# Optimization experiments

Measured on AMD Instinct MI355X. Metric: run time of the kernel, lower is better.

## Reference

```python
import jax, jax.numpy as jnp
import numpy as np

# dims
B, S = 1, 32768          # batch, grid seqlen (32^3 latent grid)
NQ, NE = 32768, 262144   # mesh query nodes, grid->query edges
IN, EMB, HID, BOT, PREDH, OUT, NDIM = 192, 192, 192, 192, 192, 4, 3
MAX_WAVELENGTH = 10000.0


def sincos_embed(coords, dim, ndim):
    # ContinuousSincosEmbed: dim % ndim == 0 and (dim//ndim) even here -> no padding
    eff = dim // ndim                                     # 64 dims per coordinate
    omega = 1.0 / MAX_WAVELENGTH ** (jnp.arange(0, eff, 2, dtype=jnp.float32) / eff)  # [eff//2]
    out = coords[..., None] * omega                       # [N, ndim, eff//2]
    emb = jnp.concatenate([jnp.sin(out), jnp.cos(out)], axis=-1)  # [N, ndim, eff]
    return emb.reshape(coords.shape[0], ndim * eff)       # [N, dim]


def _linear_params(key, fan_in, fan_out):
    k1, k2 = jax.random.split(key)
    lim = 1.0 / np.sqrt(fan_in)
    w = jax.random.uniform(k1, (fan_in, fan_out), jnp.float32, -lim, lim)
    b = jax.random.uniform(k2, (fan_out,), jnp.float32, -lim, lim)
    return w, b


def setup_inputs() -> dict:
    key = jax.random.key(0)
    ks = jax.random.split(key, 10)
    x = jax.random.normal(ks[0], (B, S, IN), jnp.float32)
    query_pos = jax.random.uniform(ks[1], (NQ, NDIM), jnp.float32) * 100.0
    # edges sorted by query index (required by the CSR segment reduce in the original)
    qidx = jnp.sort(jax.random.randint(ks[2], (NE,), 0, NQ))
    gidx = jax.random.randint(ks[3], (NE,), 0, B * S)
    grid_to_query_edges = jnp.stack([qidx, gidx], axis=1).astype(jnp.int64)
    proj_w, proj_b = _linear_params(ks[4], IN, EMB)
    msg0_w, msg0_b = _linear_params(ks[5], 2 * EMB, 2 * HID)
    msg1_w, msg1_b = _linear_params(ks[6], 2 * HID, 2 * HID)
    msg2_w, msg2_b = _linear_params(ks[7], 2 * HID, BOT)
    pred0_w, pred0_b = _linear_params(ks[8], BOT, PREDH)
    pred1_w, pred1_b = _linear_params(ks[9], PREDH, OUT)
    return dict(x=x, query_pos=query_pos, grid_to_query_edges=grid_to_query_edges,
                proj_w=proj_w, proj_b=proj_b,
                msg0_w=msg0_w, msg0_b=msg0_b, msg1_w=msg1_w, msg1_b=msg1_b,
                msg2_w=msg2_w, msg2_b=msg2_b,
                pred0_w=pred0_w, pred0_b=pred0_b, pred1_w=pred1_w, pred1_b=pred1_b)


def reference(x, query_pos, grid_to_query_edges,
              proj_w, proj_b, msg0_w, msg0_b, msg1_w, msg1_b, msg2_w, msg2_b,
              pred0_w, pred0_b, pred1_w, pred1_b):
    gelu = lambda t: jax.nn.gelu(t, approximate=False)  # torch nn.GELU default (erf)
    # flatten grid tokens and project
    xf = x.reshape(-1, x.shape[-1]) @ proj_w + proj_b          # [B*S, EMB]
    qe = sincos_embed(query_pos, EMB, NDIM)                    # [NQ, EMB]
    qidx = grid_to_query_edges[:, 0]
    gidx = grid_to_query_edges[:, 1]
    # gather + concat per edge
    h = jnp.concatenate([xf[gidx], qe[qidx]], axis=1)          # [NE, 2*EMB]
    # message MLP
    h = gelu(h @ msg0_w + msg0_b)
    h = gelu(h @ msg1_w + msg1_b)
    h = h @ msg2_w + msg2_b                                    # [NE, BOT]
    # segment mean to query nodes (empty segments -> 0, matching segment_csr mean)
    nq = query_pos.shape[0]
    seg_sum = jax.ops.segment_sum(h, qidx, num_segments=nq)    # [NQ, BOT]
    cnt = jax.ops.segment_sum(jnp.ones((qidx.shape[0], 1), h.dtype), qidx, num_segments=nq)
    m = seg_sum / jnp.maximum(cnt, 1.0)
    # prediction head
    out = gelu(m @ pred0_w + pred0_b) @ pred1_w + pred1_b      # [NQ, OUT]
    return out
```

## Files before the change

### kernel.cpp

```cpp
#include <hip/hip_runtime.h>
#include <math.h>

#define N_Q    32768
#define N_E    262144

typedef _Float16 half8 __attribute__((ext_vector_type(8)));
typedef _Float16 half4v __attribute__((ext_vector_type(4)));
typedef float f32x4 __attribute__((ext_vector_type(4)));

__device__ __forceinline__ float gelu_f(float x) {
    float ax = fabsf(x);
    float t = __builtin_amdgcn_rcpf(fmaf(0.33269070724668f, ax, 1.0f));
    float poly = t * fmaf(t, fmaf(t, 0.7478556f, -0.0958798f), 0.3480242f);
    float e = exp2f(-0.72134752044448f * ax * ax);
    float u = fmaf(-poly, e, 1.0f);
    return 0.5f * fmaf(ax, u, x);
}

__global__ __launch_bounds__(256) void embed_kernel(const float* __restrict__ qpos,
                                                    _Float16* __restrict__ qe) {
    int gid = blockIdx.x * 256 + threadIdx.x;
    int q = gid / 96, r = gid - q * 96;
    int d = r >> 5, i = r & 31;
    float omega = exp2f(-(float)i * 0.41524101186092029f);
    float arg = qpos[q * 3 + d] * omega;
    float rev = arg * 0.15915494309189535f;
    rev = rev - floorf(rev);
    float s = __builtin_amdgcn_sinf(rev);
    float c = __builtin_amdgcn_cosf(rev);
    int base = q * 192 + d * 64 + i;
    qe[base] = (_Float16)s;
    qe[base + 32] = (_Float16)c;
}

__device__ __forceinline__ void pack_one(const float* __restrict__ W,
                                         _Float16* __restrict__ Wp,
                                         int K, int N, int blk0, int tid) {
    int u = blk0 * 256 + tid;
    if (u * 8 >= K * N) return;
    int l = u & 63, blk = u >> 6;
    int nks = K >> 5;
    int ntile = blk / nks, ks = blk - ntile * nks;
    int n = ntile * 16 + (l & 15);
    int k0 = ks * 32 + (l >> 4) * 8;
    half8 v;
    #pragma unroll
    for (int j = 0; j < 8; ++j) v[j] = (_Float16)W[(size_t)(k0 + j) * N + n];
    *(half8*)(Wp + (size_t)u * 8) = v;
}

__global__ __launch_bounds__(256) void pack_all_kernel(
    const float* __restrict__ pw,  _Float16* __restrict__ WpP,
    const float* __restrict__ m0,  _Float16* __restrict__ Wp0,
    const float* __restrict__ m1,  _Float16* __restrict__ Wp1,
    const float* __restrict__ m2,  _Float16* __restrict__ Wp2,
    const float* __restrict__ hw,  _Float16* __restrict__ WpH) {
    int b = blockIdx.x, t = threadIdx.x;
    if      (b < 18)  pack_one(pw, WpP, 192, 192, b,        t);
    else if (b < 90)  pack_one(m0, Wp0, 384, 384, b - 18,   t);
    else if (b < 162) pack_one(m1, Wp1, 384, 384, b - 90,   t);
    else if (b < 198) pack_one(m2, Wp2, 384, 192, b - 162,  t);
    else              pack_one(hw, WpH, 192, 192, b - 198,  t);
}

#define PK 200

__global__ __launch_bounds__(256, 2) void proj_mfma_kernel(
    const float* __restrict__ x, const _Float16* __restrict__ Wp,
    const float* __restrict__ bias, _Float16* __restrict__ xf)
{
    __shared__ _Float16 hA[64 * PK];
    const int t = threadIdx.x;
    const int r0 = blockIdx.x * 64;
    const int lane = t & 63;
    const int w = t >> 6;
    const int ln = lane & 15, lq = lane >> 4;

    #pragma unroll
    for (int i = 0; i < 12; ++i) {
        int idx = t + 256 * i;
        int r = idx / 48, c4 = idx - r * 48;
        float4 v = ((const float4*)(x + (size_t)(r0 + r) * 192))[c4];
        half4v hv; hv[0] = (_Float16)v.x; hv[1] = (_Float16)v.y;
        hv[2] = (_Float16)v.z; hv[3] = (_Float16)v.w;
        *(half4v*)(hA + r * PK + c4 * 4) = hv;
    }
    __syncthreads();

    f32x4 acc[4][3];
    #pragma unroll
    for (int nt = 0; nt < 3; ++nt) {
        float bv = bias[w * 48 + nt * 16 + ln];
        #pragma unroll
        for (int mt = 0; mt < 4; ++mt) acc[mt][nt] = (f32x4){bv, bv, bv, bv};
    }
    #pragma unroll 2
    for (int ks = 0; ks < 6; ++ks) {
        half8 a[4], bf[3];
        #pragma unroll
        for (int mt = 0; mt < 4; ++mt)
            a[mt] = *(const half8*)(hA + (mt * 16 + ln) * PK + ks * 32 + lq * 8);
        #pragma unroll
        for (int nt = 0; nt < 3; ++nt)
            bf[nt] = *(const half8*)(Wp + (size_t)(((w * 3 + nt) * 6 + ks) * 512 + lane * 8));
        #pragma unroll
        for (int nt = 0; nt < 3; ++nt)
            #pragma unroll
            for (int mt = 0; mt < 4; ++mt)
                acc[mt][nt] = __builtin_amdgcn_mfma_f32_16x16x32_f16(a[mt], bf[nt], acc[mt][nt], 0, 0, 0);
    }
    #pragma unroll
    for (int mt = 0; mt < 4; ++mt)
        #pragma unroll
        for (int nt = 0; nt < 3; ++nt)
            #pragma unroll
            for (int r = 0; r < 4; ++r) {
                int m = mt * 16 + lq * 4 + r;
                int n = w * 48 + nt * 16 + ln;
                xf[(size_t)(r0 + m) * 192 + n] = (_Float16)acc[mt][nt][r];
            }
}

#define PADK 392

__global__ __launch_bounds__(512, 6) void edge_mlp_kernel(
    const _Float16* __restrict__ xf, const _Float16* __restrict__ qe,
    const int* __restrict__ edges,
    const _Float16* __restrict__ Wp0, const float* __restrict__ b0,
    const _Float16* __restrict__ Wp1, const float* __restrict__ b1,
    const _Float16* __restrict__ Wp2, const float* __restrict__ b2,
    float* __restrict__ seg, float* __restrict__ cnt)
{
    __shared__ _Float16 hA[64 * PADK];
    __shared__ int qi[64], gi[64];
    float* h2 = (float*)hA;

    const int t = threadIdx.x;
    const int e0 = blockIdx.x * 64;
    const int lane = t & 63;
    const int w = t >> 6;
    const int ln = lane & 15;
    const int lq = lane >> 4;

    if (t < 64) {
        qi[t] = edges[2 * (e0 + t)];
        gi[t] = edges[2 * (e0 + t) + 1];
    }
    __syncthreads();

    #pragma unroll
    for (int i = 0; i < 6; ++i) {
        int idx = t + 512 * i;
        int m = idx / 48, c = idx - m * 48;
        const half8* src = (c < 24) ? ((const half8*)(xf + (size_t)gi[m] * 192) + c)
                                    : ((const half8*)(qe + (size_t)qi[m] * 192) + (c - 24));
        *(half8*)(hA + m * PADK + c * 8) = *src;
    }
    __syncthreads();

    #pragma unroll 1
    for (int L = 0; L < 2; ++L) {
        const _Float16* __restrict__ Wp = L ? Wp1 : Wp0;
        const float* __restrict__ bias = L ? b1 : b0;

        f32x4 acc[4][3];
        #pragma unroll
        for (int nt = 0; nt < 3; ++nt) {
            float bv = bias[w * 48 + nt * 16 + ln];
            #pragma unroll
            for (int mt = 0; mt < 4; ++mt)
                acc[mt][nt] = (f32x4){bv, bv, bv, bv};
        }
        #pragma unroll 2
        for (int ks = 0; ks < 12; ++ks) {
            half8 a[4], bf[3];
            #pragma unroll
            for (int mt = 0; mt < 4; ++mt)
                a[mt] = *(const half8*)(hA + (mt * 16 + ln) * PADK + ks * 32 + lq * 8);
            #pragma unroll
            for (int nt = 0; nt < 3; ++nt)
                bf[nt] = *(const half8*)(Wp + (size_t)(((w * 3 + nt) * 12 + ks) * 512 + lane * 8));
            #pragma unroll
            for (int nt = 0; nt < 3; ++nt)
                #pragma unroll
                for (int mt = 0; mt < 4; ++mt)
                    acc[mt][nt] = __builtin_amdgcn_mfma_f32_16x16x32_f16(a[mt], bf[nt], acc[mt][nt], 0, 0, 0);
        }
        __syncthreads();
        #pragma unroll
        for (int mt = 0; mt < 4; ++mt)
            #pragma unroll
            for (int nt = 0; nt < 3; ++nt)
                #pragma unroll
                for (int r = 0; r < 4; ++r) {
                    int m = mt * 16 + lq * 4 + r;
                    int n = w * 48 + nt * 16 + ln;
                    hA[m * PADK + n] = (_Float16)gelu_f(acc[mt][nt][r]);
                }
        __syncthreads();
    }

    {
        const int n0 = (w & 3) * 48;
        const int mh = (w >> 2) * 2;
        f32x4 acc[2][3];
        #pragma unroll
        for (int nt = 0; nt < 3; ++nt) {
            float bv = b2[n0 + nt * 16 + ln];
            #pragma unroll
            for (int mt = 0; mt < 2; ++mt)
                acc[mt][nt] = (f32x4){bv, bv, bv, bv};
        }
        #pragma unroll 2
        for (int ks = 0; ks < 12; ++ks) {
            half8 a[2], bf[3];
            #pragma unroll
            for (int mt = 0; mt < 2; ++mt)
                a[mt] = *(const half8*)(hA + ((mh + mt) * 16 + ln) * PADK + ks * 32 + lq * 8);
            #pragma unroll
            for (int nt = 0; nt < 3; ++nt)
                bf[nt] = *(const half8*)(Wp2 + (size_t)((((w & 3) * 3 + nt) * 12 + ks) * 512 + lane * 8));
            #pragma unroll
            for (int nt = 0; nt < 3; ++nt)
                #pragma unroll
                for (int mt = 0; mt < 2; ++mt)
                    acc[mt][nt] = __builtin_amdgcn_mfma_f32_16x16x32_f16(a[mt], bf[nt], acc[mt][nt], 0, 0, 0);
        }
        __syncthreads();
        #pragma unroll
        for (int mt = 0; mt < 2; ++mt)
            #pragma unroll
            for (int nt = 0; nt < 3; ++nt)
                #pragma unroll
                for (int r = 0; r < 4; ++r) {
                    int m = (mh + mt) * 16 + lq * 4 + r;
                    int n = n0 + nt * 16 + ln;
                    h2[m * 192 + n] = acc[mt][nt][r];
                }
        __syncthreads();
    }

    if (t < 384) {
        int half = t >= 192;
        int col = t - half * 192;
        int mlo = half * 32, mhi = mlo + 32;
        float a = 0.0f;
        for (int m = mlo; m < mhi; ++m) {
            a += h2[m * 192 + col];
            if (m == mhi - 1 || qi[m + 1] != qi[m]) {
                atomicAdd(&seg[(size_t)qi[m] * 192 + col], a);
                a = 0.0f;
            }
        }
    } else if (t < 386) {
        int half = t - 384;
        int mlo = half * 32, mhi = mlo + 32;
        float run = 1.0f;
        for (int m = mlo + 1; m < mhi; ++m) {
            if (qi[m] != qi[m - 1]) { atomicAdd(&cnt[qi[m - 1]], run); run = 1.0f; }
            else run += 1.0f;
        }
        atomicAdd(&cnt[qi[mhi - 1]], run);
    }
}

#define PSK 196

__global__ __launch_bounds__(256, 2) void head_kernel(
    const float* __restrict__ seg, const float* __restrict__ cnt,
    const _Float16* __restrict__ Wp0, const float* __restrict__ b0,
    const float* __restrict__ w1, const float* __restrict__ b1,
    float* __restrict__ out)
{
    __shared__ _Float16 hA[64 * PK];
    __shared__ float ps[64 * PSK];
    __shared__ float w1s[192 * 4];
    __shared__ float invc[64];
    const int t = threadIdx.x;
    const int r0 = blockIdx.x * 64;
    const int lane = t & 63;
    const int w = t >> 6;
    const int ln = lane & 15, lq = lane >> 4;

    if (t < 64) invc[t] = 1.0f / fmaxf(cnt[r0 + t], 1.0f);
    if (t < 192) ((float4*)w1s)[t] = ((const float4*)w1)[t];
    __syncthreads();

    #pragma unroll
    for (int i = 0; i < 12; ++i) {
        int idx = t + 256 * i;
        int r = idx / 48, c4 = idx - r * 48;
        float inv = invc[r];
        float4 v = ((const float4*)(seg + (size_t)(r0 + r) * 192))[c4];
        half4v hv; hv[0] = (_Float16)(v.x * inv); hv[1] = (_Float16)(v.y * inv);
        hv[2] = (_Float16)(v.z * inv); hv[3] = (_Float16)(v.w * inv);
        *(half4v*)(hA + r * PK + c4 * 4) = hv;
    }
    __syncthreads();

    f32x4 acc[4][3];
    #pragma unroll
    for (int nt = 0; nt < 3; ++nt) {
        float bv = b0[w * 48 + nt * 16 + ln];
        #pragma unroll
        for (int mt = 0; mt < 4; ++mt) acc[mt][nt] = (f32x4){bv, bv, bv, bv};
    }
    #pragma unroll 2
    for (int ks = 0; ks < 6; ++ks) {
        half8 a[4], bf[3];
        #pragma unroll
        for (int mt = 0; mt < 4; ++mt)
            a[mt] = *(const half8*)(hA + (mt * 16 + ln) * PK + ks * 32 + lq * 8);
        #pragma unroll
        for (int nt = 0; nt < 3; ++nt)
            bf[nt] = *(const half8*)(Wp0 + (size_t)(((w * 3 + nt) * 6 + ks) * 512 + lane * 8));
        #pragma unroll
        for (int nt = 0; nt < 3; ++nt)
            #pragma unroll
            for (int mt = 0; mt < 4; ++mt)
                acc[mt][nt] = __builtin_amdgcn_mfma_f32_16x16x32_f16(a[mt], bf[nt], acc[mt][nt], 0, 0, 0);
    }
    #pragma unroll
    for (int mt = 0; mt < 4; ++mt)
        #pragma unroll
        for (int nt = 0; nt < 3; ++nt)
            #pragma unroll
            for (int r = 0; r < 4; ++r) {
                int m = mt * 16 + lq * 4 + r;
                int n = w * 48 + nt * 16 + ln;
                ps[m * PSK + n] = gelu_f(acc[mt][nt][r]);
            }
    __syncthreads();

    {
        int r = t >> 2, oo = t & 3;
        float a = b1[oo];
        for (int k = 0; k < 192; ++k)
            a = fmaf(ps[r * PSK + k], w1s[k * 4 + oo], a);
        out[(size_t)(r0 + r) * 4 + oo] = a;
    }
}

extern "C" void kernel_launch(void* const* d_in, const int* in_sizes, int n_in,
                              void* d_out, int out_size, void* d_ws, size_t ws_size,
                              hipStream_t stream) {
    (void)in_sizes; (void)n_in; (void)out_size; (void)ws_size;
    const float* x       = (const float*)d_in[0];
    const float* qpos    = (const float*)d_in[1];
    const int*   edges   = (const int*)d_in[2];
    const float* proj_w  = (const float*)d_in[3];
    const float* proj_b  = (const float*)d_in[4];
    const float* msg0_w  = (const float*)d_in[5];
    const float* msg0_b  = (const float*)d_in[6];
    const float* msg1_w  = (const float*)d_in[7];
    const float* msg1_b  = (const float*)d_in[8];
    const float* msg2_w  = (const float*)d_in[9];
    const float* msg2_b  = (const float*)d_in[10];
    const float* pred0_w = (const float*)d_in[11];
    const float* pred0_b = (const float*)d_in[12];
    const float* pred1_w = (const float*)d_in[13];
    const float* pred1_b = (const float*)d_in[14];
    float* out = (float*)d_out;

    char* ws = (char*)d_ws;
    _Float16* xf  = (_Float16*)(ws);
    _Float16* qe  = (_Float16*)(ws + 12582912);
    float*    seg = (float*)(ws + 25165824);
    float*    cnt = (float*)(ws + 50331648);
    _Float16* Wp0 = (_Float16*)(ws + 50462720);
    _Float16* Wp1 = (_Float16*)(ws + 50757632);
    _Float16* Wp2 = (_Float16*)(ws + 51052544);
    _Float16* WpP = (_Float16*)(ws + 51200000);
    _Float16* WpH = (_Float16*)(ws + 51273728);

    hipMemsetAsync(seg, 0, 25165824 + 131072, stream);
    embed_kernel<<<12288, 256, 0, stream>>>(qpos, qe);
    pack_all_kernel<<<216, 256, 0, stream>>>(proj_w, WpP, msg0_w, Wp0,
                                             msg1_w, Wp1, msg2_w, Wp2,
                                             pred0_w, WpH);
    proj_mfma_kernel<<<512, 256, 0, stream>>>(x, WpP, proj_b, xf);
    edge_mlp_kernel<<<4096, 512, 0, stream>>>(xf, qe, edges,
                                              Wp0, msg0_b, Wp1, msg1_b, Wp2, msg2_b,
                                              seg, cnt);
    head_kernel<<<512, 256, 0, stream>>>(seg, cnt, WpH, pred0_b,
                                         pred1_w, pred1_b, out);
}
```

Measured before the change: 372.4 us.

## Fuse prep launches, restructure edge gather, hoist address math, vectorise head dot

Merges the sincos embedding, weight packing and segment-buffer zeroing into a single prep kernel, replacing a memset and two launches. Rewrites the edge-feature gather so each thread copies strided 16-byte chunks of one edge's grid and query rows. Precomputes LDS and weight base pointers in the MFMA loops and epilogues, and vectorises the head's final 192-wide dot product with float4 reads. Intent is to cut launch overhead and per-iteration index arithmetic; the gather layout change may alter coalescing behaviour.

```diff
diff --git a/kernel.cpp b/kernel.cpp
--- a/kernel.cpp
+++ b/kernel.cpp
@@ -15,22 +15,6 @@
     float e = exp2f(-0.72134752044448f * ax * ax);
     float u = fmaf(-poly, e, 1.0f);
     return 0.5f * fmaf(ax, u, x);
-}
-
-__global__ __launch_bounds__(256) void embed_kernel(const float* __restrict__ qpos,
-                                                    _Float16* __restrict__ qe) {
-    int gid = blockIdx.x * 256 + threadIdx.x;
-    int q = gid / 96, r = gid - q * 96;
-    int d = r >> 5, i = r & 31;
-    float omega = exp2f(-(float)i * 0.41524101186092029f);
-    float arg = qpos[q * 3 + d] * omega;
-    float rev = arg * 0.15915494309189535f;
-    rev = rev - floorf(rev);
-    float s = __builtin_amdgcn_sinf(rev);
-    float c = __builtin_amdgcn_cosf(rev);
-    int base = q * 192 + d * 64 + i;
-    qe[base] = (_Float16)s;
-    qe[base + 32] = (_Float16)c;
 }
 
 __device__ __forceinline__ void pack_one(const float* __restrict__ W,
@@ -49,18 +33,43 @@
     *(half8*)(Wp + (size_t)u * 8) = v;
 }
 
-__global__ __launch_bounds__(256) void pack_all_kernel(
+__global__ __launch_bounds__(256) void prep_kernel(
+    const float* __restrict__ qpos, _Float16* __restrict__ qe,
     const float* __restrict__ pw,  _Float16* __restrict__ WpP,
     const float* __restrict__ m0,  _Float16* __restrict__ Wp0,
     const float* __restrict__ m1,  _Float16* __restrict__ Wp1,
     const float* __restrict__ m2,  _Float16* __restrict__ Wp2,
-    const float* __restrict__ hw,  _Float16* __restrict__ WpH) {
-    int b = blockIdx.x, t = threadIdx.x;
-    if      (b < 18)  pack_one(pw, WpP, 192, 192, b,        t);
-    else if (b < 90)  pack_one(m0, Wp0, 384, 384, b - 18,   t);
-    else if (b < 162) pack_one(m1, Wp1, 384, 384, b - 90,   t);
-    else if (b < 198) pack_one(m2, Wp2, 384, 192, b - 162,  t);
-    else              pack_one(hw, WpH, 192, 192, b - 198,  t);
+    const float* __restrict__ hw,  _Float16* __restrict__ WpH,
+    float* __restrict__ segz)
+{
+    const int b = blockIdx.x, t = threadIdx.x;
+    if (b < 12288) {
+        int gid = b * 256 + t;
+        int q = gid / 96, r = gid - q * 96;
+        int d = r >> 5, i = r & 31;
+        float omega = exp2f(-(float)i * 0.41524101186092029f);
+        float arg = qpos[q * 3 + d] * omega;
+        float rev = arg * 0.15915494309189535f;
+        rev = rev - floorf(rev);
+        float s = __builtin_amdgcn_sinf(rev);
+        float c = __builtin_amdgcn_cosf(rev);
+        int base = q * 192 + d * 64 + i;
+        qe[base] = (_Float16)s;
+        qe[base + 32] = (_Float16)c;
+    } else if (b < 12504) {
+        int bb = b - 12288;
+        if      (bb < 18)  pack_one(pw, WpP, 192, 192, bb,       t);
+        else if (bb < 90)  pack_one(m0, Wp0, 384, 384, bb - 18,  t);
+        else if (bb < 162) pack_one(m1, Wp1, 384, 384, bb - 90,  t);
+        else if (bb < 198) pack_one(m2, Wp2, 384, 192, bb - 162, t);
+        else               pack_one(hw, WpH, 192, 192, bb - 198, t);
+    } else {
+        int idx = (b - 12504) * 256 + t;
+        float4 z = make_float4(0.f, 0.f, 0.f, 0.f);
+        #pragma unroll
+        for (int j = 0; j < 4; ++j)
+            ((float4*)segz)[idx + j * 395264] = z;
+    }
 }
 
 #define PK 200
@@ -94,12 +103,13 @@
         #pragma unroll
         for (int mt = 0; mt < 4; ++mt) acc[mt][nt] = (f32x4){bv, bv, bv, bv};
     }
+    const _Float16* abase = hA + ln * PK + lq * 8;
     #pragma unroll 2
     for (int ks = 0; ks < 6; ++ks) {
         half8 a[4], bf[3];
         #pragma unroll
         for (int mt = 0; mt < 4; ++mt)
-            a[mt] = *(const half8*)(hA + (mt * 16 + ln) * PK + ks * 32 + lq * 8);
+            a[mt] = *(const half8*)(abase + mt * 16 * PK + ks * 32);
         #pragma unroll
         for (int nt = 0; nt < 3; ++nt)
             bf[nt] = *(const half8*)(Wp + (size_t)(((w * 3 + nt) * 6 + ks) * 512 + lane * 8));
@@ -148,21 +158,33 @@
     }
     __syncthreads();
 
-    #pragma unroll
-    for (int i = 0; i < 6; ++i) {
-        int idx = t + 512 * i;
-        int m = idx / 48, c = idx - m * 48;
-        const half8* src = (c < 24) ? ((const half8*)(xf + (size_t)gi[m] * 192) + c)
-                                    : ((const half8*)(qe + (size_t)qi[m] * 192) + (c - 24));
-        *(half8*)(hA + m * PADK + c * 8) = *src;
-    }
-    __syncthreads();
+    {
+        const int gm = t >> 3;
+        const int sub = t & 7;
+        const half8* xsrc = (const half8*)(xf + (size_t)gi[gm] * 192) + sub;
+        const half8* qsrc = (const half8*)(qe + (size_t)qi[gm] * 192) + sub;
+        _Float16* dst = hA + gm * PADK + sub * 8;
+        #pragma unroll
+        for (int i = 0; i < 3; ++i)
+            *(half8*)(dst + i * 64) = xsrc[i * 8];
+        #pragma unroll
+        for (int i = 0; i < 3; ++i)
+            *(half8*)(dst + 192 + i * 64) = qsrc[i * 8];
+    }
+    __syncthreads();
+
+    const _Float16* abase = hA + ln * PADK + lq * 8;
 
     #pragma unroll 1
     for (int L = 0; L < 2; ++L) {
         const _Float16* __restrict__ Wp = L ? Wp1 : Wp0;
         const float* __restrict__ bias = L ? b1 : b0;
 
+        const _Float16* wb[3];
+        #pragma unroll
+        for (int nt = 0; nt < 3; ++nt)
+            wb[nt] = Wp + (size_t)((w * 3 + nt) * 12) * 512 + lane * 8;
+
         f32x4 acc[4][3];
         #pragma unroll
         for (int nt = 0; nt < 3; ++nt) {
@@ -176,10 +198,10 @@
             half8 a[4], bf[3];
             #pragma unroll
             for (int mt = 0; mt < 4; ++mt)
-                a[mt] = *(const half8*)(hA + (mt * 16 + ln) * PADK + ks * 32 + lq * 8);
-            #pragma unroll
-            for (int nt = 0; nt < 3; ++nt)
-                bf[nt] = *(const half8*)(Wp + (size_t)(((w * 3 + nt) * 12 + ks) * 512 + lane * 8));
+                a[mt] = *(const half8*)(abase + mt * 16 * PADK + ks * 32);
+            #pragma unroll
+            for (int nt = 0; nt < 3; ++nt)
+                bf[nt] = *(const half8*)(wb[nt] + ks * 512);
             #pragma unroll
             for (int nt = 0; nt < 3; ++nt)
                 #pragma unroll
@@ -187,22 +209,25 @@
                     acc[mt][nt] = __builtin_amdgcn_mfma_f32_16x16x32_f16(a[mt], bf[nt], acc[mt][nt], 0, 0, 0);
         }
         __syncthreads();
+        _Float16* wbase = hA + (lq * 4) * PADK + w * 48 + ln;
         #pragma unroll
         for (int mt = 0; mt < 4; ++mt)
             #pragma unroll
             for (int nt = 0; nt < 3; ++nt)
                 #pragma unroll
-                for (int r = 0; r < 4; ++r) {
-                    int m = mt * 16 + lq * 4 + r;
-                    int n = w * 48 + nt * 16 + ln;
-                    hA[m * PADK + n] = (_Float16)gelu_f(acc[mt][nt][r]);
-                }
+                for (int r = 0; r < 4; ++r)
+                    wbase[(mt * 16 + r) * PADK + nt * 16] = (_Float16)gelu_f(acc[mt][nt][r]);
         __syncthreads();
     }
 
     {
         const int n0 = (w & 3) * 48;
         const int mh = (w >> 2) * 2;
+        const _Float16* wb[3];
+        #pragma unroll
+        for (int nt = 0; nt < 3; ++nt)
+            wb[nt] = Wp2 + (size_t)(((w & 3) * 3 + nt) * 12) * 512 + lane * 8;
+
         f32x4 acc[2][3];
         #pragma unroll
         for (int nt = 0; nt < 3; ++nt) {
@@ -211,15 +236,16 @@
             for (int mt = 0; mt < 2; ++mt)
                 acc[mt][nt] = (f32x4){bv, bv, bv, bv};
         }
+        const _Float16* abase2 = hA + (mh * 16 + ln) * PADK + lq * 8;
         #pragma unroll 2
         for (int ks = 0; ks < 12; ++ks) {
             half8 a[2], bf[3];
             #pragma unroll
             for (int mt = 0; mt < 2; ++mt)
-                a[mt] = *(const half8*)(hA + ((mh + mt) * 16 + ln) * PADK + ks * 32 + lq * 8);
-            #pragma unroll
-            for (int nt = 0; nt < 3; ++nt)
-                bf[nt] = *(const half8*)(Wp2 + (size_t)((((w & 3) * 3 + nt) * 12 + ks) * 512 + lane * 8));
+                a[mt] = *(const half8*)(abase2 + mt * 16 * PADK + ks * 32);
+            #pragma unroll
+            for (int nt = 0; nt < 3; ++nt)
+                bf[nt] = *(const half8*)(wb[nt] + ks * 512);
             #pragma unroll
             for (int nt = 0; nt < 3; ++nt)
                 #pragma unroll
@@ -227,16 +253,14 @@
                     acc[mt][nt] = __builtin_amdgcn_mfma_f32_16x16x32_f16(a[mt], bf[nt], acc[mt][nt], 0, 0, 0);
         }
         __syncthreads();
+        float* sbase = h2 + (mh * 16 + lq * 4) * 192 + n0 + ln;
         #pragma unroll
         for (int mt = 0; mt < 2; ++mt)
             #pragma unroll
             for (int nt = 0; nt < 3; ++nt)
                 #pragma unroll
-                for (int r = 0; r < 4; ++r) {
-                    int m = (mh + mt) * 16 + lq * 4 + r;
-                    int n = n0 + nt * 16 + ln;
-                    h2[m * 192 + n] = acc[mt][nt][r];
-                }
+                for (int r = 0; r < 4; ++r)
+                    sbase[(mt * 16 + r) * 192 + nt * 16] = acc[mt][nt][r];
         __syncthreads();
     }
 
@@ -305,12 +329,13 @@
         #pragma unroll
         for (int mt = 0; mt < 4; ++mt) acc[mt][nt] = (f32x4){bv, bv, bv, bv};
     }
+    const _Float16* abase = hA + ln * PK + lq * 8;
     #pragma unroll 2
     for (int ks = 0; ks < 6; ++ks) {
         half8 a[4], bf[3];
         #pragma unroll
         for (int mt = 0; mt < 4; ++mt)
-            a[mt] = *(const half8*)(hA + (mt * 16 + ln) * PK + ks * 32 + lq * 8);
+            a[mt] = *(const half8*)(abase + mt * 16 * PK + ks * 32);
         #pragma unroll
         for (int nt = 0; nt < 3; ++nt)
             bf[nt] = *(const half8*)(Wp0 + (size_t)(((w * 3 + nt) * 6 + ks) * 512 + lane * 8));
@@ -335,8 +360,15 @@
     {
         int r = t >> 2, oo = t & 3;
         float a = b1[oo];
-        for (int k = 0; k < 192; ++k)
-            a = fmaf(ps[r * PSK + k], w1s[k * 4 + oo], a);
+        const float4* prow = (const float4*)(ps + r * PSK);
+        #pragma unroll 4
+        for (int k4 = 0; k4 < 48; ++k4) {
+            float4 v = prow[k4];
+            a = fmaf(v.x, w1s[(k4 * 4 + 0) * 4 + oo], a);
+            a = fmaf(v.y, w1s[(k4 * 4 + 1) * 4 + oo], a);
+            a = fmaf(v.z, w1s[(k4 * 4 + 2) * 4 + oo], a);
+            a = fmaf(v.w, w1s[(k4 * 4 + 3) * 4 + oo], a);
+        }
         out[(size_t)(r0 + r) * 4 + oo] = a;
     }
 }
@@ -373,11 +405,9 @@
     _Float16* WpP = (_Float16*)(ws + 51200000);
     _Float16* WpH = (_Float16*)(ws + 51273728);
 
-    hipMemsetAsync(seg, 0, 25165824 + 131072, stream);
-    embed_kernel<<<12288, 256, 0, stream>>>(qpos, qe);
-    pack_all_kernel<<<216, 256, 0, stream>>>(proj_w, WpP, msg0_w, Wp0,
-                                             msg1_w, Wp1, msg2_w, Wp2,
-                                             pred0_w, WpH);
+    prep_kernel<<<14048, 256, 0, stream>>>(qpos, qe, proj_w, WpP,
+                                           msg0_w, Wp0, msg1_w, Wp1,
+                                           msg2_w, Wp2, pred0_w, WpH, seg);
     proj_mfma_kernel<<<512, 256, 0, stream>>>(x, WpP, proj_b, xf);
     edge_mlp_kernel<<<4096, 512, 0, stream>>>(xf, qe, edges,
                                               Wp0, msg0_b, Wp1, msg1_b, Wp2, msg2_b,
```

Measured after the change: 382.1 us. +2.6%, slower.
